# Kernel tuning notes

Hardware: AMD Instinct MI355X
Metric: run time of the kernel (lower is better)

Reference implementation:

```python
import jax, jax.numpy as jnp
import numpy as np

GAMMA_NEG = 4.0
GAMMA_POS = 1.0
CLIP = 0.05
EPS = 1e-08
ALPHA3 = 2.0
TOPK = 10
B, C = 4096, 9605


def setup_inputs() -> dict:
    key = jax.random.key(0)
    k1, k2, k3, k4, k5, k6 = jax.random.split(key, 6)
    x = jax.random.normal(k1, (B, C), dtype=jnp.float32)
    y = (jax.random.uniform(k2, (B, C)) < 0.02).astype(jnp.float32)
    whitelist_mask = jax.random.randint(k3, (C,), 0, 100) == 0
    compost_idx = jax.random.randint(k4, (70,), 0, C, dtype=jnp.int32)
    recycle_idx = jax.random.randint(k5, (70,), 0, C, dtype=jnp.int32)
    donate_idx = jax.random.randint(k6, (70,), 0, C, dtype=jnp.int32)
    return {"x": x, "y": y, "whitelist_mask": whitelist_mask,
            "compost_idx": compost_idx, "recycle_idx": recycle_idx,
            "donate_idx": donate_idx}


def reference(x, y, whitelist_mask, compost_idx, recycle_idx, donate_idx):
    xs_pos = jax.nn.sigmoid(x)                       # [B, C]
    xs_neg = jnp.minimum(1.0 - xs_pos + CLIP, 1.0)   # asymmetric clipping
    # base binary cross-entropy (positive log term, clamped)
    loss = (y * jnp.log(jnp.maximum(xs_pos, EPS))
            + (1.0 - y) * jnp.log(jnp.maximum(xs_neg, EPS)))

    # per-sample: does ground truth hit any whitelist (compost/recycle/donate)?
    wl_idx = jnp.concatenate([compost_idx, recycle_idx, donate_idx])  # [210]
    gt_none = jnp.sum(y[:, wl_idx], axis=1) == 0.0    # [B] -> gt_whitelist == [4]

    # top-10 predictions per sample (argsort descending, first 10)
    _, top10 = jax.lax.top_k(xs_pos, TOPK)            # [B, 10]
    y_top = jnp.take_along_axis(y, top10, axis=1)     # [B, 10]
    wl_top = whitelist_mask[top10]                    # [B, 10]
    # non-whitelisted class: penalize iff gt hits no whitelist
    # whitelisted class:     penalize iff y[i, index] == 0
    penalize = jnp.where(wl_top, y_top == 0.0, gt_none[:, None])  # [B, 10]
    mult_vals = jnp.where(penalize, ALPHA3, 1.0)      # [B, 10]
    rows = jnp.arange(x.shape[0])[:, None]
    mult = jnp.ones_like(loss).at[rows, top10].set(mult_vals)
    loss = loss * mult

    # asymmetric focal weighting (no grad through the weight)
    pt = xs_pos * y + xs_neg * (1.0 - y)
    one_sided_gamma = GAMMA_POS * y + GAMMA_NEG * (1.0 - y)
    one_sided_w = jax.lax.stop_gradient(jnp.power(1.0 - pt, one_sided_gamma))
    loss = loss * one_sided_w
    return -jnp.sum(loss)
```

## Files before the change

kernel.cpp:

```cpp
#include <hip/hip_runtime.h>
#include <stdint.h>

#define B_DIM 4096
#define C_DIM 9605
#define NT 512
#define NW (NT / 64)
#define VEC_N 8192
#define TOPK_N 10
#define CAP 1024
#define EPS_F 1e-8f
#define LOG2E_F 1.4426950408889634f
#define LN2_D 0.6931471805599453
#define CLIP_F 0.05f
#define XTHRESH 2.5f

typedef float f4a __attribute__((ext_vector_type(4), aligned(16)));

__device__ __forceinline__ float sigmoid_f(float x) {
  float e = __builtin_amdgcn_exp2f(-x * LOG2E_F);
  return __builtin_amdgcn_rcpf(1.0f + e);
}

__device__ __forceinline__ float loss2_term(float s, bool pos) {
  float xn = fminf(1.0f + CLIP_F - s, 1.0f);
  float z = pos ? fmaxf(s, EPS_F) : fmaxf(xn, EPS_F);
  float logz = __builtin_amdgcn_logf(z);
  float t = fmaxf(s - CLIP_F, 0.0f);
  float t2 = t * t;
  float w = pos ? (1.0f - s) : (t2 * t2);
  return logz * w;
}

__device__ __forceinline__ unsigned long long make_key(float s, int c, bool pos) {
  return ((unsigned long long)__float_as_uint(s) << 15)
       | (unsigned long long)(((uint32_t)(c ^ 0x3FFF) << 1) | (pos ? 1u : 0u));
}

__device__ __forceinline__ void process_elem(float xval, float yval, int c,
                                             float& lsum,
                                             unsigned long long* cand, int* cnt) {
  float s = sigmoid_f(xval);
  bool pos = (yval != 0.0f);
  lsum += loss2_term(s, pos);
  if (xval > XTHRESH) {
    int slot = atomicAdd(cnt, 1);
    unsigned long long key = make_key(s, c, pos);
    if (slot < CAP) cand[slot] = key;
  }
}

__global__ __launch_bounds__(NT, 8) void asym_loss_row_kernel(
    const float* __restrict__ x, const float* __restrict__ y,
    const unsigned char* __restrict__ wl_mask,
    const int* __restrict__ compost, const int* __restrict__ recycle,
    const int* __restrict__ donate, float* __restrict__ row_out) {
  __shared__ unsigned long long cand[CAP];
  __shared__ float s_part[NW];
  __shared__ int s_cnt;
  __shared__ int s_gtany;

  const int row = blockIdx.x;
  const int tid = threadIdx.x;
  const int lane = tid & 63;
  const int wid = tid >> 6;
  const float* xr = x + (size_t)row * C_DIM;
  const float* yr = y + (size_t)row * C_DIM;

  if (tid == 0) { s_cnt = 0; s_gtany = 0; }
  __syncthreads();

  if (tid < 210) {
    int idx = (tid < 70) ? compost[tid]
            : (tid < 140) ? recycle[tid - 70]
                          : donate[tid - 140];
    if (yr[idx] != 0.0f) atomicOr(&s_gtany, 1);
  }

  const int a = (4 - (row & 3)) & 3;
  float lsum = 0.0f;

  if (tid < a) process_elem(xr[tid], yr[tid], tid, lsum, cand, &s_cnt);

  const float* xa = xr + a;
  const float* ya = yr + a;
  f4a xv[4], yv[4];
#pragma unroll
  for (int k = 0; k < 4; ++k) {
    int c4 = (k * NT + tid) * 4;
    xv[k] = *(const f4a*)(xa + c4);
    yv[k] = *(const f4a*)(ya + c4);
  }
#pragma unroll
  for (int k = 0; k < 4; ++k) {
    int c4 = a + (k * NT + tid) * 4;
#pragma unroll
    for (int j = 0; j < 4; ++j)
      process_elem(xv[k][j], yv[k][j], c4 + j, lsum, cand, &s_cnt);
  }
  for (int c = a + VEC_N + tid; c < C_DIM; c += NT)
    process_elem(xr[c], yr[c], c, lsum, cand, &s_cnt);

#pragma unroll
  for (int off = 32; off; off >>= 1) lsum += __shfl_xor(lsum, off, 64);
  if (lane == 0) s_part[wid] = lsum;
  __syncthreads();

  if (wid == 0) {
    const int n = s_cnt;
    const bool gt_none = (s_gtany == 0);
    unsigned long long prev = ~0ull;
    unsigned long long mykey = 0ull;

    if (n >= TOPK_N && n <= CAP) {
#pragma unroll 1
      for (int r = 0; r < TOPK_N; ++r) {
        unsigned long long loc = 0ull;
        for (int i = lane; i < n; i += 64) {
          unsigned long long k = cand[i];
          if (k < prev && k > loc) loc = k;
        }
#pragma unroll
        for (int off = 32; off; off >>= 1) {
          unsigned long long o = __shfl_xor(loc, off, 64);
          loc = loc > o ? loc : o;
        }
        if (lane == r) mykey = loc;
        prev = loc;
      }
    } else {
#pragma unroll 1
      for (int r = 0; r < TOPK_N; ++r) {
        unsigned long long loc = 0ull;
        for (int i = lane; i < C_DIM; i += 64) {
          float s = sigmoid_f(xr[i]);
          unsigned long long k = make_key(s, i, yr[i] != 0.0f);
          if (k < prev && k > loc) loc = k;
        }
#pragma unroll
        for (int off = 32; off; off >>= 1) {
          unsigned long long o = __shfl_xor(loc, off, 64);
          loc = loc > o ? loc : o;
        }
        if (lane == r) mykey = loc;
        prev = loc;
      }
    }

    float extra = 0.0f;
    if (lane < TOPK_N) {
      int wc = 0x3FFF ^ (int)((mykey >> 1) & 0x3FFFull);
      bool ypos = (mykey & 1ull) != 0ull;
      float s = __uint_as_float((uint32_t)(mykey >> 15));
      bool wl = (wl_mask[wc] != 0);
      bool pen = wl ? (!ypos) : gt_none;
      if (pen) extra = loss2_term(s, ypos);
    }
#pragma unroll
    for (int off = 32; off; off >>= 1) extra += __shfl_xor(extra, off, 64);
    if (lane == 0) {
      float tot = extra;
#pragma unroll
      for (int w2 = 0; w2 < NW; ++w2) tot += s_part[w2];
      row_out[row] = tot;
    }
  }
}

__global__ void finalize_kernel(const float* __restrict__ row_out,
                                float* __restrict__ out) {
  const int tid = threadIdx.x;
  const int lane = tid & 63;
  const int wid = tid >> 6;
  __shared__ double sp[4];
  double acc = 0.0;
  for (int i = tid; i < B_DIM; i += 256) acc += (double)row_out[i];
#pragma unroll
  for (int off = 32; off; off >>= 1) acc += __shfl_down(acc, off, 64);
  if (lane == 0) sp[wid] = acc;
  __syncthreads();
  if (tid == 0) {
    double t = sp[0] + sp[1] + sp[2] + sp[3];
    out[0] = (float)(-t * LN2_D);
  }
}

extern "C" void kernel_launch(void* const* d_in, const int* in_sizes, int n_in,
                              void* d_out, int out_size, void* d_ws, size_t ws_size,
                              hipStream_t stream) {
  (void)in_sizes; (void)n_in; (void)out_size; (void)ws_size;
  const float* x = (const float*)d_in[0];
  const float* y = (const float*)d_in[1];
  const unsigned char* wl = (const unsigned char*)d_in[2];
  const int* compost = (const int*)d_in[3];
  const int* recycle = (const int*)d_in[4];
  const int* donate  = (const int*)d_in[5];
  float* row_part = (float*)d_ws;

  asym_loss_row_kernel<<<B_DIM, NT, 0, stream>>>(x, y, wl, compost, recycle,
                                                 donate, row_part);
  finalize_kernel<<<1, 256, 0, stream>>>(row_part, (float*)d_out);
}
```

Before: 66.34 us.

## Fuse final reduction into row kernel via last-block counter, halve block size

Drops the separate finalize kernel: each block bumps a global counter after writing its row sum, and the last block to finish does the cross-row reduction. A memset is added to reset the counter on each call. The block size drops from 512 to 256 threads, with each thread now loading 8 vector chunks of x and y in flight instead of 4, which raises register pressure. The EPS clamps inside the log are also removed.

Result: slower. 246.2 us (+271.2%).

```diff
diff --git a/kernel.cpp b/kernel.cpp
--- a/kernel.cpp
+++ b/kernel.cpp
@@ -3,14 +3,14 @@
 
 #define B_DIM 4096
 #define C_DIM 9605
-#define NT 512
+#define NT 256
 #define NW (NT / 64)
-#define VEC_N 8192
+#define CHUNKS 8
+#define VEC_N (NT * 4 * CHUNKS)
 #define TOPK_N 10
 #define CAP 1024
-#define EPS_F 1e-8f
 #define LOG2E_F 1.4426950408889634f
-#define LN2_D 0.6931471805599453
+#define LN2_F 0.6931471805599453f
 #define CLIP_F 0.05f
 #define XTHRESH 2.5f
 
@@ -23,7 +23,7 @@
 
 __device__ __forceinline__ float loss2_term(float s, bool pos) {
   float xn = fminf(1.0f + CLIP_F - s, 1.0f);
-  float z = pos ? fmaxf(s, EPS_F) : fmaxf(xn, EPS_F);
+  float z = pos ? s : xn;
   float logz = __builtin_amdgcn_logf(z);
   float t = fmaxf(s - CLIP_F, 0.0f);
   float t2 = t * t;
@@ -44,20 +44,21 @@
   lsum += loss2_term(s, pos);
   if (xval > XTHRESH) {
     int slot = atomicAdd(cnt, 1);
-    unsigned long long key = make_key(s, c, pos);
-    if (slot < CAP) cand[slot] = key;
-  }
-}
-
-__global__ __launch_bounds__(NT, 8) void asym_loss_row_kernel(
+    if (slot < CAP) cand[slot] = make_key(s, c, pos);
+  }
+}
+
+__global__ __launch_bounds__(NT, 5) void asym_loss_row_kernel(
     const float* __restrict__ x, const float* __restrict__ y,
     const unsigned char* __restrict__ wl_mask,
     const int* __restrict__ compost, const int* __restrict__ recycle,
-    const int* __restrict__ donate, float* __restrict__ row_out) {
+    const int* __restrict__ donate, unsigned int* __restrict__ done_cnt,
+    float* __restrict__ row_out, float* __restrict__ out) {
   __shared__ unsigned long long cand[CAP];
   __shared__ float s_part[NW];
   __shared__ int s_cnt;
   __shared__ int s_gtany;
+  __shared__ int s_last;
 
   const int row = blockIdx.x;
   const int tid = threadIdx.x;
@@ -78,24 +79,24 @@
 
   const int a = (4 - (row & 3)) & 3;
   float lsum = 0.0f;
-
   if (tid < a) process_elem(xr[tid], yr[tid], tid, lsum, cand, &s_cnt);
 
   const float* xa = xr + a;
   const float* ya = yr + a;
-  f4a xv[4], yv[4];
-#pragma unroll
-  for (int k = 0; k < 4; ++k) {
+  f4a X[CHUNKS], Y[CHUNKS];
+#pragma unroll
+  for (int k = 0; k < CHUNKS; ++k) {
     int c4 = (k * NT + tid) * 4;
-    xv[k] = *(const f4a*)(xa + c4);
-    yv[k] = *(const f4a*)(ya + c4);
-  }
-#pragma unroll
-  for (int k = 0; k < 4; ++k) {
+    X[k] = *(const f4a*)(xa + c4);
+    Y[k] = *(const f4a*)(ya + c4);
+  }
+  asm volatile("" ::: "memory");
+#pragma unroll
+  for (int k = 0; k < CHUNKS; ++k) {
     int c4 = a + (k * NT + tid) * 4;
 #pragma unroll
     for (int j = 0; j < 4; ++j)
-      process_elem(xv[k][j], yv[k][j], c4 + j, lsum, cand, &s_cnt);
+      process_elem(X[k][j], Y[k][j], c4 + j, lsum, cand, &s_cnt);
   }
   for (int c = a + VEC_N + tid; c < C_DIM; c += NT)
     process_elem(xr[c], yr[c], c, lsum, cand, &s_cnt);
@@ -161,26 +162,31 @@
       float tot = extra;
 #pragma unroll
       for (int w2 = 0; w2 < NW; ++w2) tot += s_part[w2];
-      row_out[row] = tot;
-    }
-  }
-}
-
-__global__ void finalize_kernel(const float* __restrict__ row_out,
-                                float* __restrict__ out) {
-  const int tid = threadIdx.x;
-  const int lane = tid & 63;
-  const int wid = tid >> 6;
-  __shared__ double sp[4];
-  double acc = 0.0;
-  for (int i = tid; i < B_DIM; i += 256) acc += (double)row_out[i];
-#pragma unroll
-  for (int off = 32; off; off >>= 1) acc += __shfl_down(acc, off, 64);
-  if (lane == 0) sp[wid] = acc;
+      row_out[row] = tot * LN2_F;
+    }
+  }
+
+  if (tid == 0) {
+    __threadfence();
+    unsigned int old = atomicAdd(done_cnt, 1u);
+    s_last = (old == (unsigned)(B_DIM - 1)) ? 1 : 0;
+  }
   __syncthreads();
-  if (tid == 0) {
-    double t = sp[0] + sp[1] + sp[2] + sp[3];
-    out[0] = (float)(-t * LN2_D);
+  if (s_last) {
+    __threadfence();
+    double acc = 0.0;
+    for (int i = tid; i < B_DIM; i += NT) acc += (double)row_out[i];
+#pragma unroll
+    for (int off = 32; off; off >>= 1) acc += __shfl_down(acc, off, 64);
+    __shared__ double sp[NW];
+    if (lane == 0) sp[wid] = acc;
+    __syncthreads();
+    if (tid == 0) {
+      double t = 0.0;
+#pragma unroll
+      for (int w2 = 0; w2 < NW; ++w2) t += sp[w2];
+      out[0] = (float)(-t);
+    }
   }
 }
 
@@ -194,9 +200,12 @@
   const int* compost = (const int*)d_in[3];
   const int* recycle = (const int*)d_in[4];
   const int* donate  = (const int*)d_in[5];
-  float* row_part = (float*)d_ws;
-
+
+  unsigned int* done_cnt = (unsigned int*)d_ws;
+  float* row_part = (float*)d_ws + 4;
+
+  hipMemsetAsync(done_cnt, 0, sizeof(unsigned int), stream);
   asym_loss_row_kernel<<<B_DIM, NT, 0, stream>>>(x, y, wl, compost, recycle,
-                                                 donate, row_part);
-  finalize_kernel<<<1, 256, 0, stream>>>(row_part, (float*)d_out);
-}
+                                                 donate, done_cnt, row_part,
+                                                 (float*)d_out);
+}
```
